# Optimization experiments

Measured on AMD Instinct MI355X. Metric: run time of the kernel, lower is better.

## Reference

```python
import jax, jax.numpy as jnp
import numpy as np
from math import factorial, sqrt

CUTOFF = 5.0
MAX_BASIS_DEG = 2   # degrees in bond basis expansion
MAX_DEG = 4         # degrees in atomic descriptors and output
N_ATOMS = 20000
N_EDGES = 50000
F = 16              # num radial features


def _fac(n):
    return factorial(n)


def _cg(j1, m1, j2, m2, j3, m3):
    # complex Clebsch-Gordan coefficient (Racah formula), small integer l's
    if m1 + m2 != m3:
        return 0.0
    if j3 < abs(j1 - j2) or j3 > j1 + j2:
        return 0.0
    pre = sqrt((2*j3+1) * _fac(j3+j1-j2) * _fac(j3-j1+j2) * _fac(j1+j2-j3) / _fac(j1+j2+j3+1))
    pre *= sqrt(_fac(j3+m3)*_fac(j3-m3)*_fac(j1-m1)*_fac(j1+m1)*_fac(j2-m2)*_fac(j2+m2))
    s = 0.0
    for k in range(max(0, j2-j3-m1, j1-j3+m2), min(j1+j2-j3, j1-m1, j2+m2) + 1):
        s += (-1)**k / (_fac(k)*_fac(j1+j2-j3-k)*_fac(j1-m1-k)*_fac(j2+m2-k)*_fac(j3-j2+m1+k)*_fac(j3-j1-m2+k))
    return pre * s


def _umat(l):
    # complex -> real spherical harmonic change of basis, rows real m (-l..l), cols complex mu
    U = np.zeros((2*l+1, 2*l+1), dtype=np.complex128)
    s2 = 1.0 / np.sqrt(2.0)
    for m in range(-l, l+1):
        if m > 0:
            U[m+l, m+l] = ((-1)**m) * s2
            U[m+l, -m+l] = s2
        elif m == 0:
            U[l, l] = 1.0
        else:
            am = -m
            U[m+l, m+l] = 1j * s2
            U[m+l, am+l] = -1j * ((-1)**am) * s2
    return U


def _real_cg(l1, l2, l3):
    C = np.zeros((2*l1+1, 2*l2+1, 2*l3+1), dtype=np.complex128)
    for m1 in range(-l1, l1+1):
        for m2 in range(-l2, l2+1):
            m3 = m1 + m2
            if -l3 <= m3 <= l3:
                C[m1+l1, m2+l2, m3+l3] = _cg(l1, m1, l2, m2, l3, m3)
    G = np.einsum('aA,bB,cC,ABC->abc', _umat(l1), _umat(l2), np.conj(_umat(l3)), C)
    G = G.real if (l1 + l2 + l3) % 2 == 0 else G.imag
    return G.astype(np.float32)


# selection-rule-allowed coupling paths (l1 from bond basis, l2 from atom features, l3 output)
PATHS = [(l1, l2, l3)
         for l1 in range(MAX_BASIS_DEG + 1)
         for l2 in range(MAX_DEG + 1)
         for l3 in range(abs(l1 - l2), min(l1 + l2, MAX_DEG) + 1)]
CG_BLOCKS = [jnp.asarray(_real_cg(*p)) for p in PATHS]


def _real_sh_l2(u):
    # real spherical harmonics up to l=2, m order -l..l (cartesian_order=False)
    x, y, z = u[..., 0], u[..., 1], u[..., 2]
    c1 = 0.4886025119029199
    c2 = 1.0925484305920792
    return jnp.stack([
        jnp.full_like(x, 0.28209479177387814),
        c1*y, c1*z, c1*x,
        c2*x*y, c2*y*z, 0.31539156525252005*(3.0*z*z - 1.0), c2*x*z, 0.5*c2*(x*x - y*y),
    ], axis=-1)


def _forward(atomic_descriptors, tp_weights, neighbour_displacements, neighbour_indices):
    # gather atom-pair descriptors and add -> bond-centered features (E,1,25,F)
    y = atomic_descriptors[neighbour_indices[:, 0]] + atomic_descriptors[neighbour_indices[:, 1]]
    r = jnp.linalg.norm(neighbour_displacements, axis=-1)
    u = neighbour_displacements / jnp.maximum(r, 1e-9)[:, None]
    sh = _real_sh_l2(u)                                    # (E, 9)
    k = jnp.arange(1, F + 1, dtype=jnp.float32)
    rad = jnp.sinc(k[None, :] * (r / CUTOFF)[:, None])     # jinc-like radial basis, zero at cutoff
    rad = jnp.where((r < CUTOFF)[:, None], rad, 0.0)       # (E, F)
    bond = rad[:, None, :] * sh[:, :, None]                # (E, 9, F)
    E = y.shape[0]
    out = jnp.zeros((E, 2, (MAX_DEG + 1)**2, F), dtype=jnp.float32)
    for p, (l1, l2, l3) in enumerate(PATHS):
        a = bond[:, l1*l1:(l1+1)**2, :]                    # (E, 2l1+1, F)
        b = y[:, 0, l2*l2:(l2+1)**2, :]                    # (E, 2l2+1, F)
        contrib = jnp.einsum('eaf,ebf,abc->ecf', a, b, CG_BLOCKS[p]) * tp_weights[p][None, None, :]
        out = out.at[:, (l1 + l2 + l3) % 2, l3*l3:(l3+1)**2, :].add(contrib)
    return out


def setup_inputs() -> dict:
    key = jax.random.key(0)
    k1, k2, k3, k4 = jax.random.split(key, 4)
    atomic_descriptors = jax.random.normal(k1, (N_ATOMS, 1, (MAX_DEG + 1)**2, F), dtype=jnp.float32)
    neighbour_indices = jax.random.randint(k2, (N_EDGES, 2), 0, N_ATOMS)
    neighbour_displacements = jax.random.normal(k3, (N_EDGES, 3), dtype=jnp.float32) * 1.5
    tp_weights = jax.random.normal(k4, (len(PATHS), F), dtype=jnp.float32) * 0.1
    return {
        'atomic_descriptors': atomic_descriptors,
        'tp_weights': tp_weights,
        'neighbour_displacements': neighbour_displacements,
        'neighbour_indices': neighbour_indices,
    }


def reference(atomic_descriptors, tp_weights, neighbour_displacements, neighbour_indices):
    return _forward(atomic_descriptors, tp_weights, neighbour_displacements, neighbour_indices)
```

## Files before the change

kernel.cpp:

```cpp
#include <hip/hip_runtime.h>
#include <utility>
#include <cstddef>

#define N_ATOMS 20000
#define N_EDGES 50000
#define FDIM 16
#define NPATHS 33

namespace cgx {

constexpr double cfac(int n){ double r = 1.0; for (int i = 2; i <= n; ++i) r *= (double)i; return r; }

constexpr double csqrt(double x){
  if (x <= 0.0) return 0.0;
  double g = (x >= 1.0) ? x : 1.0;
  for (int i = 0; i < 200; ++i){
    double ng = 0.5 * (g + x / g);
    if (ng == g) break;
    g = ng;
  }
  return g;
}

constexpr double cg_coef(int j1,int m1,int j2,int m2,int j3,int m3){
  if (m1 + m2 != m3) return 0.0;
  int dlo = (j1 > j2) ? (j1 - j2) : (j2 - j1);
  if (j3 < dlo || j3 > j1 + j2) return 0.0;
  double pre = csqrt((2.0*j3+1.0) * cfac(j3+j1-j2) * cfac(j3-j1+j2) * cfac(j1+j2-j3) / cfac(j1+j2+j3+1));
  pre *= csqrt(cfac(j3+m3)*cfac(j3-m3)*cfac(j1-m1)*cfac(j1+m1)*cfac(j2-m2)*cfac(j2+m2));
  int kmin = 0;
  if (j2 - j3 - m1 > kmin) kmin = j2 - j3 - m1;
  if (j1 - j3 + m2 > kmin) kmin = j1 - j3 + m2;
  int kmax = j1 + j2 - j3;
  if (j1 - m1 < kmax) kmax = j1 - m1;
  if (j2 + m2 < kmax) kmax = j2 + m2;
  double s = 0.0;
  for (int k = kmin; k <= kmax; ++k){
    double t = 1.0 / (cfac(k)*cfac(j1+j2-j3-k)*cfac(j1-m1-k)*cfac(j2+m2-k)*cfac(j3-j2+m1+k)*cfac(j3-j1-m2+k));
    s += (k & 1) ? -t : t;
  }
  return pre * s;
}

struct Cplx { double re; double im; };
constexpr double S2C = 0.70710678118654752440;

constexpr Cplx u_entry(int l, int row, int col){
  int m = row - l;
  if (m > 0){
    if (col == m + l)  return Cplx{ (m & 1) ? -S2C : S2C, 0.0 };
    if (col == -m + l) return Cplx{ S2C, 0.0 };
  } else if (m == 0){
    if (col == l) return Cplx{ 1.0, 0.0 };
  } else {
    int am = -m;
    if (col == m + l)  return Cplx{ 0.0, S2C };
    if (col == am + l) return Cplx{ 0.0, (am & 1) ? S2C : -S2C };
  }
  return Cplx{ 0.0, 0.0 };
}

template<int L1,int L2,int L3>
struct CGCTab { double v[(2*L1+1)*(2*L2+1)]; };

template<int L1,int L2,int L3>
constexpr CGCTab<L1,L2,L3> make_cgc(){
  CGCTab<L1,L2,L3> t{};
  for (int A = 0; A < 2*L1+1; ++A){
    for (int B = 0; B < 2*L2+1; ++B){
      int MA = A - L1, MB = B - L2, MC = MA + MB;
      t.v[A*(2*L2+1)+B] = (MC < -L3 || MC > L3) ? 0.0 : cg_coef(L1,MA,L2,MB,L3,MC);
    }
  }
  return t;
}
template<int L1,int L2,int L3>
struct CGCH { static constexpr CGCTab<L1,L2,L3> t = make_cgc<L1,L2,L3>(); };

template<int L1,int L2,int L3>
struct GTab { float v[(2*L1+1)*(2*L2+1)*(2*L3+1)]; };

template<int L1,int L2,int L3>
constexpr GTab<L1,L2,L3> make_g(){
  GTab<L1,L2,L3> g{};
  constexpr int NA = 2*L1+1, NB = 2*L2+1, NC = 2*L3+1;
  for (int a = 0; a < NA; ++a){
    for (int b = 0; b < NB; ++b){
      for (int c = 0; c < NC; ++c){
        double re = 0.0, im = 0.0;
        for (int A = 0; A < NA; ++A){
          Cplx u1 = u_entry(L1, a, A);
          if (u1.re == 0.0 && u1.im == 0.0) continue;
          int MA = A - L1;
          for (int B = 0; B < NB; ++B){
            Cplx u2 = u_entry(L2, b, B);
            if (u2.re == 0.0 && u2.im == 0.0) continue;
            int MB = B - L2;
            int MC = MA + MB;
            if (MC < -L3 || MC > L3) continue;
            Cplx u3 = u_entry(L3, c, MC + L3);
            if (u3.re == 0.0 && u3.im == 0.0) continue;
            double cgv = CGCH<L1,L2,L3>::t.v[A*NB + B];
            if (cgv == 0.0) continue;
            u3.im = -u3.im;
            double pr = u1.re*u2.re - u1.im*u2.im;
            double pi_ = u1.re*u2.im + u1.im*u2.re;
            re += (pr*u3.re - pi_*u3.im) * cgv;
            im += (pr*u3.im + pi_*u3.re) * cgv;
          }
        }
        g.v[(a*NB + b)*NC + c] = (float)(((L1 + L2 + L3) % 2 == 0) ? re : im);
      }
    }
  }
  return g;
}
template<int L1,int L2,int L3>
struct GH { static constexpr GTab<L1,L2,L3> t = make_g<L1,L2,L3>(); };

struct PathD { int l1, l2, l3; };
constexpr PathD PATHS_C[NPATHS] = {
  {0,0,0},{0,1,1},{0,2,2},{0,3,3},{0,4,4},
  {1,0,1},{1,1,0},{1,1,1},{1,1,2},{1,2,1},{1,2,2},{1,2,3},{1,3,2},{1,3,3},{1,3,4},{1,4,3},{1,4,4},
  {2,0,2},{2,1,1},{2,1,2},{2,1,3},{2,2,0},{2,2,1},{2,2,2},{2,2,3},{2,2,4},
  {2,3,1},{2,3,2},{2,3,3},{2,3,4},{2,4,2},{2,4,3},{2,4,4}
};

constexpr const float* G_PTRS[NPATHS] = {
  GH<0,0,0>::t.v, GH<0,1,1>::t.v, GH<0,2,2>::t.v, GH<0,3,3>::t.v, GH<0,4,4>::t.v,
  GH<1,0,1>::t.v, GH<1,1,0>::t.v, GH<1,1,1>::t.v, GH<1,1,2>::t.v, GH<1,2,1>::t.v,
  GH<1,2,2>::t.v, GH<1,2,3>::t.v, GH<1,3,2>::t.v, GH<1,3,3>::t.v, GH<1,3,4>::t.v,
  GH<1,4,3>::t.v, GH<1,4,4>::t.v,
  GH<2,0,2>::t.v, GH<2,1,1>::t.v, GH<2,1,2>::t.v, GH<2,1,3>::t.v, GH<2,2,0>::t.v,
  GH<2,2,1>::t.v, GH<2,2,2>::t.v, GH<2,2,3>::t.v, GH<2,2,4>::t.v, GH<2,3,1>::t.v,
  GH<2,3,2>::t.v, GH<2,3,3>::t.v, GH<2,3,4>::t.v, GH<2,4,2>::t.v, GH<2,4,3>::t.v,
  GH<2,4,4>::t.v
};

constexpr bool keep(float v){ return v > 1e-12f || v < -1e-12f; }

constexpr int count_nnz(){
  int n = 0;
  for (int p = 0; p < NPATHS; ++p){
    int l1 = PATHS_C[p].l1, l2 = PATHS_C[p].l2, l3 = PATHS_C[p].l3;
    int tot = (2*l1+1)*(2*l2+1)*(2*l3+1);
    for (int i = 0; i < tot; ++i) if (keep(G_PTRS[p][i])) ++n;
  }
  return n;
}
constexpr int NNZ = count_nnz();
static_assert(NNZ > 100 && NNZ < 4013, "unexpected CG sparsity");

struct EntryList {
  short slot[NNZ];
  short ag[NNZ];
  short bg[NNZ];
  short p[NNZ];
  float val[NNZ];
};

constexpr EntryList make_entries(){
  EntryList E{};
  int n = 0;
  for (int p = 0; p < NPATHS; ++p){
    const int l1 = PATHS_C[p].l1, l2 = PATHS_C[p].l2, l3 = PATHS_C[p].l3;
    const int NA = 2*l1+1, NB = 2*l2+1, NC = 2*l3+1;
    const int parity = (l1 + l2 + l3) & 1;
    for (int a = 0; a < NA; ++a)
      for (int b = 0; b < NB; ++b)
        for (int c = 0; c < NC; ++c){
          const float v = G_PTRS[p][(a*NB + b)*NC + c];
          if (keep(v)){
            E.slot[n] = (short)(parity*25 + l3*l3 + c);
            E.ag[n]   = (short)(l1*l1 + a);
            E.bg[n]   = (short)(l2*l2 + b);
            E.p[n]    = (short)p;
            E.val[n]  = v;
            ++n;
          }
        }
  }
  return E;
}
constexpr EntryList EN = make_entries();

}


template<int I>
__device__ __forceinline__ void apply_entry(float* __restrict__ acc, const float* __restrict__ sh,
                                            const float* __restrict__ yv, const float* __restrict__ wtp){
  constexpr int   slot = cgx::EN.slot[I];
  constexpr int   ag   = cgx::EN.ag[I];
  constexpr int   bg   = cgx::EN.bg[I];
  constexpr int   p    = cgx::EN.p[I];
  constexpr float v    = cgx::EN.val[I];
  acc[slot] += v * ((wtp[p] * sh[ag]) * yv[bg]);
}

template<std::size_t... Is>
__device__ __forceinline__ void apply_all(float* __restrict__ acc, const float* __restrict__ sh,
                                          const float* __restrict__ yv, const float* __restrict__ wtp,
                                          std::index_sequence<Is...>){
  (apply_entry<(int)Is>(acc, sh, yv, wtp), ...);
}

__global__ void __launch_bounds__(256)
BondCenteredTensorMomentDescriptor_62173946576949_kernel(
    const float* __restrict__ desc,
    const float* __restrict__ tpw,
    const float* __restrict__ disp,
    const int*   __restrict__ nidx,
    float* __restrict__ out)
{
  const int tid = blockIdx.x * 256 + threadIdx.x;
  const int f = tid & (FDIM - 1);
  const int e = tid >> 4;
  if (e >= N_EDGES) return;

  const int i0 = nidx[2*e + 0];
  const int i1 = nidx[2*e + 1];
  const float dx = disp[3*e + 0];
  const float dy = disp[3*e + 1];
  const float dz = disp[3*e + 2];

  const float r   = sqrtf(dx*dx + dy*dy + dz*dz);
  const float inv = 1.0f / fmaxf(r, 1e-9f);
  const float ux = dx*inv, uy = dy*inv, uz = dz*inv;

  float sh[9];
  sh[0] = 0.28209479177387814f;
  sh[1] = 0.4886025119029199f * uy;
  sh[2] = 0.4886025119029199f * uz;
  sh[3] = 0.4886025119029199f * ux;
  sh[4] = 1.0925484305920792f * ux * uy;
  sh[5] = 1.0925484305920792f * uy * uz;
  sh[6] = 0.31539156525252005f * (3.0f * uz * uz - 1.0f);
  sh[7] = 1.0925484305920792f * ux * uz;
  sh[8] = 0.5f * 1.0925484305920792f * (ux*ux - uy*uy);

  const float xk = (float)(f + 1) * r * 0.2f;
  const float px = 3.14159265358979323846f * xk;
  float rad = (px != 0.0f) ? (sinf(px) / px) : 1.0f;
  if (!(r < 5.0f)) rad = 0.0f;

  float wtp[NPATHS];
  #pragma unroll
  for (int p = 0; p < NPATHS; ++p) wtp[p] = rad * tpw[p * FDIM + f];

  const float* __restrict__ a0 = desc + (size_t)i0 * 400 + f;
  const float* __restrict__ a1 = desc + (size_t)i1 * 400 + f;
  float yv[25];
  #pragma unroll
  for (int b = 0; b < 25; ++b) yv[b] = a0[b * 16] + a1[b * 16];

  float acc[50];
  #pragma unroll
  for (int i = 0; i < 50; ++i) acc[i] = 0.0f;

  apply_all(acc, sh, yv, wtp, std::make_index_sequence<cgx::NNZ>{});

  float* __restrict__ op = out + (size_t)e * 800 + f;
  #pragma unroll
  for (int s = 0; s < 50; ++s) op[s * 16] = acc[s];
}

extern "C" void kernel_launch(void* const* d_in, const int* in_sizes, int n_in,
                              void* d_out, int out_size, void* d_ws, size_t ws_size,
                              hipStream_t stream) {
  const float* desc = (const float*)d_in[0];
  const float* tpw  = (const float*)d_in[1];
  const float* disp = (const float*)d_in[2];
  const int*   nidx = (const int*)d_in[3];
  float* out = (float*)d_out;

  const int total_threads = N_EDGES * FDIM;
  const int block = 256;
  const int grid = (total_threads + block - 1) / block;

  BondCenteredTensorMomentDescriptor_62173946576949_kernel<<<grid, block, 0, stream>>>(
      desc, tpw, disp, nidx, out);
}
```

Measured before the change: 204.6 us.

## Split parity outputs across two thread halves and stage gathered descriptors in LDS

Doubles the block size so that each (edge, feature) pair is handled by two threads, one per output parity. Each thread now carries only 25 accumulators and roughly half the CG entries, which lowers register pressure and shortens the serial chain per thread. Neighbour descriptor rows are gathered with float4 loads into shared memory and summed there. The radial factor is applied once at the output store, and sinf is replaced by __sinf. In exchange, the spherical-harmonic and radial setup is computed twice per pair, and the fast sine is less accurate.

```diff
diff --git a/kernel.cpp b/kernel.cpp
--- a/kernel.cpp
+++ b/kernel.cpp
@@ -6,6 +6,7 @@
 #define N_EDGES 50000
 #define FDIM 16
 #define NPATHS 33
+#define EPB 16
 
 namespace cgx {
 
@@ -139,39 +140,43 @@
 
 constexpr bool keep(float v){ return v > 1e-12f || v < -1e-12f; }
 
-constexpr int count_nnz(){
+constexpr int count_nnz_par(int parity){
   int n = 0;
   for (int p = 0; p < NPATHS; ++p){
     int l1 = PATHS_C[p].l1, l2 = PATHS_C[p].l2, l3 = PATHS_C[p].l3;
+    if (((l1 + l2 + l3) & 1) != parity) continue;
     int tot = (2*l1+1)*(2*l2+1)*(2*l3+1);
     for (int i = 0; i < tot; ++i) if (keep(G_PTRS[p][i])) ++n;
   }
   return n;
 }
-constexpr int NNZ = count_nnz();
-static_assert(NNZ > 100 && NNZ < 4013, "unexpected CG sparsity");
-
-struct EntryList {
-  short slot[NNZ];
-  short ag[NNZ];
-  short bg[NNZ];
-  short p[NNZ];
-  float val[NNZ];
+constexpr int NNZ0 = count_nnz_par(0);
+constexpr int NNZ1 = count_nnz_par(1);
+static_assert(NNZ0 > 50 && NNZ1 > 20 && NNZ0 + NNZ1 < 4013, "unexpected CG sparsity");
+
+template<int N>
+struct EListN {
+  short slot[N];
+  short ag[N];
+  short bg[N];
+  short p[N];
+  float val[N];
 };
 
-constexpr EntryList make_entries(){
-  EntryList E{};
+template<int PARITY, int N>
+constexpr EListN<N> make_entries_par(){
+  EListN<N> E{};
   int n = 0;
   for (int p = 0; p < NPATHS; ++p){
     const int l1 = PATHS_C[p].l1, l2 = PATHS_C[p].l2, l3 = PATHS_C[p].l3;
+    if (((l1 + l2 + l3) & 1) != PARITY) continue;
     const int NA = 2*l1+1, NB = 2*l2+1, NC = 2*l3+1;
-    const int parity = (l1 + l2 + l3) & 1;
     for (int a = 0; a < NA; ++a)
       for (int b = 0; b < NB; ++b)
         for (int c = 0; c < NC; ++c){
           const float v = G_PTRS[p][(a*NB + b)*NC + c];
           if (keep(v)){
-            E.slot[n] = (short)(parity*25 + l3*l3 + c);
+            E.slot[n] = (short)(l3*l3 + c);
             E.ag[n]   = (short)(l1*l1 + a);
             E.bg[n]   = (short)(l2*l2 + b);
             E.p[n]    = (short)p;
@@ -182,30 +187,37 @@
   }
   return E;
 }
-constexpr EntryList EN = make_entries();
-
-}
-
-
-template<int I>
+constexpr EListN<NNZ0> EN0 = make_entries_par<0, NNZ0>();
+constexpr EListN<NNZ1> EN1 = make_entries_par<1, NNZ1>();
+
+}
+
+
+struct Ent { int slot, ag, bg, p; float v; };
+
+template<int PAR>
+constexpr Ent get_ent(int i){
+  if constexpr (PAR == 0)
+    return Ent{ (int)cgx::EN0.slot[i], (int)cgx::EN0.ag[i], (int)cgx::EN0.bg[i], (int)cgx::EN0.p[i], cgx::EN0.val[i] };
+  else
+    return Ent{ (int)cgx::EN1.slot[i], (int)cgx::EN1.ag[i], (int)cgx::EN1.bg[i], (int)cgx::EN1.p[i], cgx::EN1.val[i] };
+}
+
+template<int PAR, int I>
 __device__ __forceinline__ void apply_entry(float* __restrict__ acc, const float* __restrict__ sh,
-                                            const float* __restrict__ yv, const float* __restrict__ wtp){
-  constexpr int   slot = cgx::EN.slot[I];
-  constexpr int   ag   = cgx::EN.ag[I];
-  constexpr int   bg   = cgx::EN.bg[I];
-  constexpr int   p    = cgx::EN.p[I];
-  constexpr float v    = cgx::EN.val[I];
-  acc[slot] += v * ((wtp[p] * sh[ag]) * yv[bg]);
-}
-
-template<std::size_t... Is>
+                                            const float* __restrict__ yv, const float* __restrict__ w){
+  constexpr Ent e = get_ent<PAR>(I);
+  acc[e.slot] += e.v * ((w[e.p] * sh[e.ag]) * yv[e.bg]);
+}
+
+template<int PAR, std::size_t... Is>
 __device__ __forceinline__ void apply_all(float* __restrict__ acc, const float* __restrict__ sh,
-                                          const float* __restrict__ yv, const float* __restrict__ wtp,
+                                          const float* __restrict__ yv, const float* __restrict__ w,
                                           std::index_sequence<Is...>){
-  (apply_entry<(int)Is>(acc, sh, yv, wtp), ...);
-}
-
-__global__ void __launch_bounds__(256)
+  (apply_entry<PAR, (int)Is>(acc, sh, yv, w), ...);
+}
+
+__global__ void __launch_bounds__(512)
 BondCenteredTensorMomentDescriptor_62173946576949_kernel(
     const float* __restrict__ desc,
     const float* __restrict__ tpw,
@@ -213,13 +225,28 @@
     const int*   __restrict__ nidx,
     float* __restrict__ out)
 {
-  const int tid = blockIdx.x * 256 + threadIdx.x;
-  const int f = tid & (FDIM - 1);
-  const int e = tid >> 4;
-  if (e >= N_EDGES) return;
-
-  const int i0 = nidx[2*e + 0];
-  const int i1 = nidx[2*e + 1];
+  __shared__ float ylds[EPB * 400];
+
+  const int e_base = blockIdx.x * EPB;
+
+  for (int q = threadIdx.x; q < EPB * 100; q += 512){
+    const int el = q / 100;
+    const int c  = q - el * 100;
+    const int e  = e_base + el;
+    const int i0 = nidx[2*e + 0];
+    const int i1 = nidx[2*e + 1];
+    const float4 a = *(const float4*)(desc + (size_t)i0 * 400 + c * 4);
+    const float4 b = *(const float4*)(desc + (size_t)i1 * 400 + c * 4);
+    float4 s; s.x = a.x + b.x; s.y = a.y + b.y; s.z = a.z + b.z; s.w = a.w + b.w;
+    *(float4*)(ylds + el * 400 + c * 4) = s;
+  }
+  __syncthreads();
+
+  const int tt = threadIdx.x & 255;
+  const int f  = tt & 15;
+  const int el = tt >> 4;
+  const int e  = e_base + el;
+
   const float dx = disp[3*e + 0];
   const float dy = disp[3*e + 1];
   const float dz = disp[3*e + 2];
@@ -239,30 +266,35 @@
   sh[7] = 1.0925484305920792f * ux * uz;
   sh[8] = 0.5f * 1.0925484305920792f * (ux*ux - uy*uy);
 
-  const float xk = (float)(f + 1) * r * 0.2f;
-  const float px = 3.14159265358979323846f * xk;
-  float rad = (px != 0.0f) ? (sinf(px) / px) : 1.0f;
+  const float px = 3.14159265358979323846f * ((float)(f + 1) * r * 0.2f);
+  float rad = (px != 0.0f) ? (__sinf(px) / px) : 1.0f;
   if (!(r < 5.0f)) rad = 0.0f;
 
-  float wtp[NPATHS];
-  #pragma unroll
-  for (int p = 0; p < NPATHS; ++p) wtp[p] = rad * tpw[p * FDIM + f];
-
-  const float* __restrict__ a0 = desc + (size_t)i0 * 400 + f;
-  const float* __restrict__ a1 = desc + (size_t)i1 * 400 + f;
   float yv[25];
   #pragma unroll
-  for (int b = 0; b < 25; ++b) yv[b] = a0[b * 16] + a1[b * 16];
-
-  float acc[50];
+  for (int b = 0; b < 25; ++b) yv[b] = ylds[el * 400 + b * 16 + f];
+
+  float acc[25];
   #pragma unroll
-  for (int i = 0; i < 50; ++i) acc[i] = 0.0f;
-
-  apply_all(acc, sh, yv, wtp, std::make_index_sequence<cgx::NNZ>{});
+  for (int i = 0; i < 25; ++i) acc[i] = 0.0f;
 
   float* __restrict__ op = out + (size_t)e * 800 + f;
-  #pragma unroll
-  for (int s = 0; s < 50; ++s) op[s * 16] = acc[s];
+
+  if (threadIdx.x < 256){
+    float w[NPATHS];
+    #pragma unroll
+    for (int p = 0; p < NPATHS; ++p) w[p] = tpw[p * FDIM + f];
+    apply_all<0>(acc, sh, yv, w, std::make_index_sequence<cgx::NNZ0>{});
+    #pragma unroll
+    for (int s = 0; s < 25; ++s) op[s * 16] = acc[s] * rad;
+  } else {
+    float w[NPATHS];
+    #pragma unroll
+    for (int p = 0; p < NPATHS; ++p) w[p] = tpw[p * FDIM + f];
+    apply_all<1>(acc, sh, yv, w, std::make_index_sequence<cgx::NNZ1>{});
+    #pragma unroll
+    for (int s = 0; s < 25; ++s) op[(25 + s) * 16] = acc[s] * rad;
+  }
 }
 
 extern "C" void kernel_launch(void* const* d_in, const int* in_sizes, int n_in,
@@ -274,10 +306,7 @@
   const int*   nidx = (const int*)d_in[3];
   float* out = (float*)d_out;
 
-  const int total_threads = N_EDGES * FDIM;
-  const int block = 256;
-  const int grid = (total_threads + block - 1) / block;
-
-  BondCenteredTensorMomentDescriptor_62173946576949_kernel<<<grid, block, 0, stream>>>(
+  const int grid = N_EDGES / EPB;
+  BondCenteredTensorMomentDescriptor_62173946576949_kernel<<<grid, 512, 0, stream>>>(
       desc, tpw, disp, nidx, out);
 }
```

Measured after the change: 259.7 us. 26.9% more time.

## Factor path weights out of CG sums and stage gathered descriptors in LDS

Applied to the files above, without the earlier changes.

The kernel now accumulates each coupling path's CG contractions into a small per-path accumulator and multiplies by the path weight once per output component, not once per nonzero. The radial factor is folded into the spherical harmonics. Neighbour descriptor rows are gathered with float4 loads into shared memory and tp weights are cached in LDS. Stores of never-touched slots become compile-time zeros and sinf becomes __sinf, which trades some accuracy for fewer FLOPs and better-coalesced gathers.

```diff
diff --git a/kernel.cpp b/kernel.cpp
--- a/kernel.cpp
+++ b/kernel.cpp
@@ -6,6 +6,7 @@
 #define N_EDGES 50000
 #define FDIM 16
 #define NPATHS 33
+#define EPB 16
 
 namespace cgx {
 
@@ -152,10 +153,9 @@
 static_assert(NNZ > 100 && NNZ < 4013, "unexpected CG sparsity");
 
 struct EntryList {
-  short slot[NNZ];
+  short c[NNZ];
   short ag[NNZ];
   short bg[NNZ];
-  short p[NNZ];
   float val[NNZ];
 };
 
@@ -165,17 +165,15 @@
   for (int p = 0; p < NPATHS; ++p){
     const int l1 = PATHS_C[p].l1, l2 = PATHS_C[p].l2, l3 = PATHS_C[p].l3;
     const int NA = 2*l1+1, NB = 2*l2+1, NC = 2*l3+1;
-    const int parity = (l1 + l2 + l3) & 1;
     for (int a = 0; a < NA; ++a)
       for (int b = 0; b < NB; ++b)
         for (int c = 0; c < NC; ++c){
           const float v = G_PTRS[p][(a*NB + b)*NC + c];
           if (keep(v)){
-            E.slot[n] = (short)(parity*25 + l3*l3 + c);
-            E.ag[n]   = (short)(l1*l1 + a);
-            E.bg[n]   = (short)(l2*l2 + b);
-            E.p[n]    = (short)p;
-            E.val[n]  = v;
+            E.c[n]  = (short)c;
+            E.ag[n] = (short)(l1*l1 + a);
+            E.bg[n] = (short)(l2*l2 + b);
+            E.val[n]= v;
             ++n;
           }
         }
@@ -184,25 +182,115 @@
 }
 constexpr EntryList EN = make_entries();
 
-}
-
-
-template<int I>
-__device__ __forceinline__ void apply_entry(float* __restrict__ acc, const float* __restrict__ sh,
-                                            const float* __restrict__ yv, const float* __restrict__ wtp){
-  constexpr int   slot = cgx::EN.slot[I];
-  constexpr int   ag   = cgx::EN.ag[I];
-  constexpr int   bg   = cgx::EN.bg[I];
-  constexpr int   p    = cgx::EN.p[I];
-  constexpr float v    = cgx::EN.val[I];
-  acc[slot] += v * ((wtp[p] * sh[ag]) * yv[bg]);
-}
-
-template<std::size_t... Is>
-__device__ __forceinline__ void apply_all(float* __restrict__ acc, const float* __restrict__ sh,
-                                          const float* __restrict__ yv, const float* __restrict__ wtp,
-                                          std::index_sequence<Is...>){
-  (apply_entry<(int)Is>(acc, sh, yv, wtp), ...);
+struct POff { int v[NPATHS + 1]; };
+constexpr POff make_poff(){
+  POff o{};
+  int n = 0;
+  o.v[0] = 0;
+  for (int p = 0; p < NPATHS; ++p){
+    const int l1 = PATHS_C[p].l1, l2 = PATHS_C[p].l2, l3 = PATHS_C[p].l3;
+    const int NA = 2*l1+1, NB = 2*l2+1, NC = 2*l3+1;
+    for (int a = 0; a < NA; ++a)
+      for (int b = 0; b < NB; ++b)
+        for (int c = 0; c < NC; ++c)
+          if (keep(G_PTRS[p][(a*NB + b)*NC + c])) ++n;
+    o.v[p + 1] = n;
+  }
+  return o;
+}
+constexpr POff POFF = make_poff();
+
+constexpr bool pacc_first(int P, int I){
+  for (int j = POFF.v[P]; j < I; ++j) if (EN.c[j] == EN.c[I]) return false;
+  return true;
+}
+constexpr bool touched(int P, int C){
+  for (int j = POFF.v[P]; j < POFF.v[P + 1]; ++j) if (EN.c[j] == C) return true;
+  return false;
+}
+constexpr int path_base(int p){
+  const int l1 = PATHS_C[p].l1, l2 = PATHS_C[p].l2, l3 = PATHS_C[p].l3;
+  return ((l1 + l2 + l3) & 1) * 25 + l3 * l3;
+}
+constexpr bool slot_first(int P, int C){
+  const int s = path_base(P) + C;
+  for (int q = 0; q < P; ++q){
+    const int b = path_base(q), nc = 2 * PATHS_C[q].l3 + 1;
+    if (s >= b && s < b + nc && touched(q, s - b)) return false;
+  }
+  return true;
+}
+constexpr bool slot_used(int s){
+  for (int q = 0; q < NPATHS; ++q){
+    const int b = path_base(q), nc = 2 * PATHS_C[q].l3 + 1;
+    if (s >= b && s < b + nc && touched(q, s - b)) return true;
+  }
+  return false;
+}
+
+}
+
+
+template<int P, int I>
+__device__ __forceinline__ void entry_op(float* __restrict__ pacc, const float* __restrict__ sh,
+                                         const float* __restrict__ yv){
+  constexpr int   c  = cgx::EN.c[I];
+  constexpr int   ag = cgx::EN.ag[I];
+  constexpr int   bg = cgx::EN.bg[I];
+  constexpr float v  = cgx::EN.val[I];
+  const float t = sh[ag] * yv[bg];
+  if constexpr (cgx::pacc_first(P, I)) pacc[c] = v * t;
+  else                                 pacc[c] += v * t;
+}
+
+template<int P, std::size_t... Is>
+__device__ __forceinline__ void path_entries(float* __restrict__ pacc, const float* __restrict__ sh,
+                                             const float* __restrict__ yv, std::index_sequence<Is...>){
+  (entry_op<P, cgx::POFF.v[P] + (int)Is>(pacc, sh, yv), ...);
+}
+
+template<int P, int C>
+__device__ __forceinline__ void path_out_one(float* __restrict__ acc, const float* __restrict__ pacc, float wp){
+  if constexpr (cgx::touched(P, C)){
+    constexpr int s = cgx::path_base(P) + C;
+    if constexpr (cgx::slot_first(P, C)) acc[s] = wp * pacc[C];
+    else                                 acc[s] += wp * pacc[C];
+  }
+}
+
+template<int P, std::size_t... Cs>
+__device__ __forceinline__ void path_out(float* __restrict__ acc, const float* __restrict__ pacc, float wp,
+                                         std::index_sequence<Cs...>){
+  (path_out_one<P, (int)Cs>(acc, pacc, wp), ...);
+}
+
+template<int P>
+__device__ __forceinline__ void apply_path(float* __restrict__ acc, const float* __restrict__ sh,
+                                           const float* __restrict__ yv, const float* __restrict__ tplds,
+                                           int f){
+  constexpr int NC = 2 * cgx::PATHS_C[P].l3 + 1;
+  float pacc[NC];
+  path_entries<P>(pacc, sh, yv, std::make_index_sequence<(std::size_t)(cgx::POFF.v[P+1] - cgx::POFF.v[P])>{});
+  const float wp = tplds[P * FDIM + f];
+  path_out<P>(acc, pacc, wp, std::make_index_sequence<NC>{});
+}
+
+template<std::size_t... Ps>
+__device__ __forceinline__ void apply_paths(float* __restrict__ acc, const float* __restrict__ sh,
+                                            const float* __restrict__ yv, const float* __restrict__ tplds,
+                                            int f, std::index_sequence<Ps...>){
+  (apply_path<(int)Ps>(acc, sh, yv, tplds, f), ...);
+}
+
+template<int S>
+__device__ __forceinline__ void store_slot(float* __restrict__ op, const float* __restrict__ acc){
+  if constexpr (cgx::slot_used(S)) op[S * FDIM] = acc[S];
+  else                             op[S * FDIM] = 0.0f;
+}
+template<std::size_t... Ss>
+__device__ __forceinline__ void store_all(float* __restrict__ op, const float* __restrict__ acc,
+                                          std::index_sequence<Ss...>){
+  (store_slot<(int)Ss>(op, acc), ...);
 }
 
 __global__ void __launch_bounds__(256)
@@ -213,56 +301,68 @@
     const int*   __restrict__ nidx,
     float* __restrict__ out)
 {
-  const int tid = blockIdx.x * 256 + threadIdx.x;
-  const int f = tid & (FDIM - 1);
-  const int e = tid >> 4;
-  if (e >= N_EDGES) return;
-
-  const int i0 = nidx[2*e + 0];
-  const int i1 = nidx[2*e + 1];
+  __shared__ float ylds[EPB * 400];
+  __shared__ float tplds[NPATHS * FDIM];
+
+  const int e_base = blockIdx.x * EPB;
+  const int tid = threadIdx.x;
+  const int f  = tid & 15;
+  const int el = tid >> 4;
+  const int e  = e_base + el;
+
+  {
+    const int i0 = nidx[2*e + 0];
+    const int i1 = nidx[2*e + 1];
+    const float* __restrict__ a0 = desc + (size_t)i0 * 400;
+    const float* __restrict__ a1 = desc + (size_t)i1 * 400;
+    #pragma unroll
+    for (int k = 0; k < 7; ++k){
+      const int c = f + 16 * k;
+      if (c < 100){
+        const float4 A = *(const float4*)(a0 + c * 4);
+        const float4 B = *(const float4*)(a1 + c * 4);
+        float4 s; s.x = A.x + B.x; s.y = A.y + B.y; s.z = A.z + B.z; s.w = A.w + B.w;
+        *(float4*)(ylds + el * 400 + c * 4) = s;
+      }
+    }
+  }
+  for (int q = tid; q < NPATHS * FDIM; q += 256) tplds[q] = tpw[q];
+  __syncthreads();
+
   const float dx = disp[3*e + 0];
   const float dy = disp[3*e + 1];
   const float dz = disp[3*e + 2];
-
   const float r   = sqrtf(dx*dx + dy*dy + dz*dz);
   const float inv = 1.0f / fmaxf(r, 1e-9f);
   const float ux = dx*inv, uy = dy*inv, uz = dz*inv;
 
+  const float px = 3.14159265358979323846f * ((float)(f + 1) * r * 0.2f);
+  float rad = (px != 0.0f) ? (__sinf(px) / px) : 1.0f;
+  if (!(r < 5.0f)) rad = 0.0f;
+
   float sh[9];
-  sh[0] = 0.28209479177387814f;
-  sh[1] = 0.4886025119029199f * uy;
-  sh[2] = 0.4886025119029199f * uz;
-  sh[3] = 0.4886025119029199f * ux;
-  sh[4] = 1.0925484305920792f * ux * uy;
-  sh[5] = 1.0925484305920792f * uy * uz;
-  sh[6] = 0.31539156525252005f * (3.0f * uz * uz - 1.0f);
-  sh[7] = 1.0925484305920792f * ux * uz;
-  sh[8] = 0.5f * 1.0925484305920792f * (ux*ux - uy*uy);
-
-  const float xk = (float)(f + 1) * r * 0.2f;
-  const float px = 3.14159265358979323846f * xk;
-  float rad = (px != 0.0f) ? (sinf(px) / px) : 1.0f;
-  if (!(r < 5.0f)) rad = 0.0f;
-
-  float wtp[NPATHS];
-  #pragma unroll
-  for (int p = 0; p < NPATHS; ++p) wtp[p] = rad * tpw[p * FDIM + f];
-
-  const float* __restrict__ a0 = desc + (size_t)i0 * 400 + f;
-  const float* __restrict__ a1 = desc + (size_t)i1 * 400 + f;
+  sh[0] = 0.28209479177387814f * rad;
+  sh[1] = (0.4886025119029199f * rad) * uy;
+  sh[2] = (0.4886025119029199f * rad) * uz;
+  sh[3] = (0.4886025119029199f * rad) * ux;
+  {
+    const float c2r = 1.0925484305920792f * rad;
+    sh[4] = c2r * ux * uy;
+    sh[5] = c2r * uy * uz;
+    sh[6] = (0.31539156525252005f * rad) * (3.0f * uz * uz - 1.0f);
+    sh[7] = c2r * ux * uz;
+    sh[8] = 0.5f * c2r * (ux*ux - uy*uy);
+  }
+
   float yv[25];
   #pragma unroll
-  for (int b = 0; b < 25; ++b) yv[b] = a0[b * 16] + a1[b * 16];
+  for (int b = 0; b < 25; ++b) yv[b] = ylds[el * 400 + b * 16 + f];
 
   float acc[50];
-  #pragma unroll
-  for (int i = 0; i < 50; ++i) acc[i] = 0.0f;
-
-  apply_all(acc, sh, yv, wtp, std::make_index_sequence<cgx::NNZ>{});
+  apply_paths(acc, sh, yv, tplds, f, std::make_index_sequence<NPATHS>{});
 
   float* __restrict__ op = out + (size_t)e * 800 + f;
-  #pragma unroll
-  for (int s = 0; s < 50; ++s) op[s * 16] = acc[s];
+  store_all(op, acc, std::make_index_sequence<50>{});
 }
 
 extern "C" void kernel_launch(void* const* d_in, const int* in_sizes, int n_in,
@@ -274,10 +374,7 @@
   const int*   nidx = (const int*)d_in[3];
   float* out = (float*)d_out;
 
-  const int total_threads = N_EDGES * FDIM;
-  const int block = 256;
-  const int grid = (total_threads + block - 1) / block;
-
-  BondCenteredTensorMomentDescriptor_62173946576949_kernel<<<grid, block, 0, stream>>>(
+  const int grid = N_EDGES / EPB;
+  BondCenteredTensorMomentDescriptor_62173946576949_kernel<<<grid, 256, 0, stream>>>(
       desc, tpw, disp, nidx, out);
 }
```

Result: no change. 206.2 us (+0.8%).
